# Kernel optimization log

Hardware: AMD Instinct MI355X
Metric: run time of the kernel (lower is better)

## Reference

```python
import jax, jax.numpy as jnp
import numpy as np
import math

NUM_LEVEL = 16
LEVEL_DIM = 2
BASE_RES = 16
LOG2_T = 19
LEVEL_SCALE = 1.38191288
N_POINTS = 262144

_PRIMES = np.array([1, 2654435761, 805459861], dtype=np.uint32)  # tiny-cuda-nn hash primes
_CORNERS = np.array([[(c >> d) & 1 for d in range(3)] for c in range(8)], dtype=np.uint32)  # [8,3]


def _grid_meta():
    # mirrors GridEncoder.get_grid_info: per-level table offsets (aligned to 8)
    max_len = 2 ** LOG2_T
    offs = []
    off = 0
    for i in range(NUM_LEVEL):
        res = int(np.ceil(BASE_RES * LEVEL_SCALE ** i))
        p = min(max_len, res ** 3)
        p = int(np.ceil(p / 8) * 8)
        offs.append(off)
        off += p
    offs.append(off)
    return offs


def setup_inputs() -> dict:
    key = jax.random.key(0)
    k1, k2 = jax.random.split(key)
    offs = _grid_meta()
    # raw coords in [-1, 1); forward maps (x+1)/2 -> [0, 1)
    input_means = jax.random.uniform(k1, (N_POINTS, 3), dtype=jnp.float32) * 2.0 - 1.0
    # embeddings.data.uniform_(-0.01, 0.01)
    embeddings = jax.random.uniform(k2, (offs[-1], LEVEL_DIM), dtype=jnp.float32) * 0.02 - 0.01
    return {"input_means": input_means, "embeddings": embeddings}


def _encode(input_means, embeddings):
    x = (input_means + 1.0) / 2.0  # [N,3] in [0,1]
    offs = _grid_meta()
    lg_scale = math.log2(LEVEL_SCALE)
    corners = jnp.asarray(_CORNERS)  # [8,3]
    primes = jnp.asarray(_PRIMES)    # [3]
    outs = []
    for l in range(NUM_LEVEL):
        hsize = offs[l + 1] - offs[l]                    # table rows this level
        scale = 2.0 ** (l * lg_scale) * BASE_RES - 1.0   # align_corners=True
        res = int(math.ceil(scale)) + 1                  # grid resolution
        table = embeddings[offs[l]:offs[l + 1]]          # [hsize, C]
        pos = x * scale                                  # align_corners -> no +0.5
        pg = jnp.floor(pos)
        frac = pos - pg                                  # [N,3]
        pgu = pg.astype(jnp.uint32)
        cpos = pgu[:, None, :] + corners[None]           # [N,8,3] corner coords
        if res ** 3 > hsize:
            # hashed level: xor of coord*prime (uint32 wraparound)
            h = cpos * primes
            idx = h[..., 0] ^ h[..., 1] ^ h[..., 2]
        else:
            # dense (tiled) level
            r = jnp.uint32(res)
            idx = cpos[..., 0] + cpos[..., 1] * r + cpos[..., 2] * r * r
        idx = (idx % jnp.uint32(hsize)).astype(jnp.int32)
        feats = table[idx]                               # [N,8,C] gather
        w = jnp.where(corners[None] == 1, frac[:, None, :], 1.0 - frac[:, None, :]).prod(-1)  # [N,8]
        outs.append(jnp.einsum('nk,nkc->nc', w, feats))  # trilinear interp
    # matches ot_encod.permute(1,0,2).reshape(N, L*C): level-major feature concat
    return jnp.concatenate(outs, axis=-1)                # [N, L*C]


def reference(input_means, embeddings):
    return _encode(input_means, embeddings)
```

## Files before the change

### kernel.cpp

```cpp
#include <hip/hip_runtime.h>
#include <cmath>

#define NPTS 262144
#define NLVL 16
#define NDENSE 5
#define NHASH 11
#define HASH_MASK 0x7FFFFu

#define PPT 2
#define CHUNK (256 * PPT)
#define CHUNKS_PER_LVL (NPTS / CHUNK)
#define TOTAL_UNITS (NHASH * CHUNKS_PER_LVL)
#define UNITS_PER_XCD (TOTAL_UNITS / 8)

typedef float vf2 __attribute__((ext_vector_type(2)));
typedef float vf4 __attribute__((ext_vector_type(4)));

struct MetaD { float scale[NDENSE]; unsigned off[NDENSE]; unsigned res[NDENSE]; };
struct MetaH { float scale[NHASH]; unsigned off[NHASH]; };

__device__ __forceinline__ vf2 hash_level(
    const float* __restrict__ emb, unsigned off, float s,
    float x, float y, float z)
{
    const float px = x * s, py = y * s, pz = z * s;
    const float gx = floorf(px), gy = floorf(py), gz = floorf(pz);
    const float fx = px - gx, fy = py - gy, fz = pz - gz;
    const unsigned ix = (unsigned)gx, iy = (unsigned)gy, iz = (unsigned)gz;

    const unsigned hy0 = iy * 2654435761u, hy1 = hy0 + 2654435761u;
    const unsigned hz0 = iz * 805459861u,  hz1 = hz0 + 805459861u;
    const unsigned hyz[4] = {hy0 ^ hz0, hy1 ^ hz0, hy0 ^ hz1, hy1 ^ hz1};

    const float wy0 = 1.0f - fy, wz0 = 1.0f - fz;
    const float wc[4] = {wy0 * wz0, fy * wz0, wy0 * fz, fy * fz};
    const float wx0 = 1.0f - fx;

    const vf2* __restrict__ emb2 = (const vf2*)emb;
    const vf4* __restrict__ emb4 = (const vf4*)emb;

    float a0 = 0.0f, a1 = 0.0f;
    if ((ix & 1u) == 0u) {
#pragma unroll
        for (int c = 0; c < 4; ++c) {
            const unsigned i0 = (ix ^ hyz[c]) & HASH_MASK;
            const vf4 f = emb4[(off + (i0 & ~1u)) >> 1];
            const bool sw = (i0 & 1u);
            const float c0x = sw ? f.z : f.x, c0y = sw ? f.w : f.y;
            const float c1x = sw ? f.x : f.z, c1y = sw ? f.y : f.w;
            a0 += wc[c] * (wx0 * c0x + fx * c1x);
            a1 += wc[c] * (wx0 * c0y + fx * c1y);
        }
    } else {
#pragma unroll
        for (int c = 0; c < 4; ++c) {
            const unsigned i0 = (ix        ^ hyz[c]) & HASH_MASK;
            const unsigned i1 = ((ix + 1u) ^ hyz[c]) & HASH_MASK;
            const vf2 f0 = emb2[off + i0];
            const vf2 f1 = emb2[off + i1];
            a0 += wc[c] * (wx0 * f0.x + fx * f1.x);
            a1 += wc[c] * (wx0 * f0.y + fx * f1.y);
        }
    }
    vf2 r; r.x = a0; r.y = a1;
    return r;
}

__global__ __launch_bounds__(256) void enc_hash(
    const float* __restrict__ means, const float* __restrict__ emb,
    float* __restrict__ dst, int lvl_major, MetaH meta)
{
    const unsigned b   = blockIdx.x;
    const unsigned g   = (b & 7u) * UNITS_PER_XCD + (b >> 3);
    const unsigned il  = g >> 9;
    const unsigned chk = g & 511u;

    const float sc     = meta.scale[il];
    const unsigned off = meta.off[il];
    const unsigned lvl = il + NDENSE;

    const unsigned p0 = chk * CHUNK + threadIdx.x;
    vf2* __restrict__ dst2 = (vf2*)dst;

#pragma unroll
    for (int pp = 0; pp < PPT; ++pp) {
        const unsigned p = p0 + (unsigned)pp * 256u;
        const float x = (means[3 * p + 0] + 1.0f) * 0.5f;
        const float y = (means[3 * p + 1] + 1.0f) * 0.5f;
        const float z = (means[3 * p + 2] + 1.0f) * 0.5f;
        const vf2 a = hash_level(emb, off, sc, x, y, z);
        if (lvl_major) {
            __builtin_nontemporal_store(a, &dst2[(size_t)il * NPTS + p]);
        } else {
            dst2[(size_t)p * NLVL + lvl] = a;
        }
    }
}

__global__ __launch_bounds__(256) void finalize(
    const float* __restrict__ means, const float* __restrict__ emb,
    const float* __restrict__ ws, float* __restrict__ out, MetaD meta)
{
    const int p = blockIdx.x * 256 + threadIdx.x;
    const vf2* __restrict__ ws2 = (const vf2*)ws;

    vf2 h0  = __builtin_nontemporal_load(&ws2[(size_t)0  * NPTS + p]);
    vf2 h1  = __builtin_nontemporal_load(&ws2[(size_t)1  * NPTS + p]);
    vf2 h2  = __builtin_nontemporal_load(&ws2[(size_t)2  * NPTS + p]);
    vf2 h3  = __builtin_nontemporal_load(&ws2[(size_t)3  * NPTS + p]);
    vf2 h4  = __builtin_nontemporal_load(&ws2[(size_t)4  * NPTS + p]);
    vf2 h5  = __builtin_nontemporal_load(&ws2[(size_t)5  * NPTS + p]);
    vf2 h6  = __builtin_nontemporal_load(&ws2[(size_t)6  * NPTS + p]);
    vf2 h7  = __builtin_nontemporal_load(&ws2[(size_t)7  * NPTS + p]);
    vf2 h8  = __builtin_nontemporal_load(&ws2[(size_t)8  * NPTS + p]);
    vf2 h9  = __builtin_nontemporal_load(&ws2[(size_t)9  * NPTS + p]);
    vf2 h10 = __builtin_nontemporal_load(&ws2[(size_t)10 * NPTS + p]);

    const float x = (means[3 * p + 0] + 1.0f) * 0.5f;
    const float y = (means[3 * p + 1] + 1.0f) * 0.5f;
    const float z = (means[3 * p + 2] + 1.0f) * 0.5f;

    const vf2* __restrict__ emb2 = (const vf2*)emb;

    vf2 d[NDENSE];
#pragma unroll
    for (int l = 0; l < NDENSE; ++l) {
        const float s      = meta.scale[l];
        const unsigned off = meta.off[l];
        const unsigned r   = meta.res[l];

        const float px = x * s, py = y * s, pz = z * s;
        const float gx = floorf(px), gy = floorf(py), gz = floorf(pz);
        const float fx = px - gx, fy = py - gy, fz = pz - gz;
        const unsigned ix = (unsigned)gx, iy = (unsigned)gy, iz = (unsigned)gz;

        const unsigned base = ix + iy * r + iz * r * r + off;
        const unsigned dy = r, dz = r * r;

        vf2 f[8];
        f[0] = emb2[base];           f[1] = emb2[base + 1];
        f[2] = emb2[base + dy];      f[3] = emb2[base + dy + 1];
        f[4] = emb2[base + dz];      f[5] = emb2[base + dz + 1];
        f[6] = emb2[base + dz + dy]; f[7] = emb2[base + dz + dy + 1];

        const float wx0 = 1.0f - fx, wy0 = 1.0f - fy, wz0 = 1.0f - fz;
        const float w00 = wz0 * wy0, w01 = wz0 * fy, w10 = fz * wy0, w11 = fz * fy;
        d[l].x = w00 * (wx0 * f[0].x + fx * f[1].x) + w01 * (wx0 * f[2].x + fx * f[3].x)
               + w10 * (wx0 * f[4].x + fx * f[5].x) + w11 * (wx0 * f[6].x + fx * f[7].x);
        d[l].y = w00 * (wx0 * f[0].y + fx * f[1].y) + w01 * (wx0 * f[2].y + fx * f[3].y)
               + w10 * (wx0 * f[4].y + fx * f[5].y) + w11 * (wx0 * f[6].y + fx * f[7].y);
    }

    float* o = out + (size_t)p * (2 * NLVL);
    vf4 v;
    v.x = d[0].x; v.y = d[0].y; v.z = d[1].x; v.w = d[1].y;
    __builtin_nontemporal_store(v, (vf4*)(o + 0));
    v.x = d[2].x; v.y = d[2].y; v.z = d[3].x; v.w = d[3].y;
    __builtin_nontemporal_store(v, (vf4*)(o + 4));
    v.x = d[4].x; v.y = d[4].y; v.z = h0.x;  v.w = h0.y;
    __builtin_nontemporal_store(v, (vf4*)(o + 8));
    v.x = h1.x; v.y = h1.y; v.z = h2.x; v.w = h2.y;
    __builtin_nontemporal_store(v, (vf4*)(o + 12));
    v.x = h3.x; v.y = h3.y; v.z = h4.x; v.w = h4.y;
    __builtin_nontemporal_store(v, (vf4*)(o + 16));
    v.x = h5.x; v.y = h5.y; v.z = h6.x; v.w = h6.y;
    __builtin_nontemporal_store(v, (vf4*)(o + 20));
    v.x = h7.x; v.y = h7.y; v.z = h8.x; v.w = h8.y;
    __builtin_nontemporal_store(v, (vf4*)(o + 24));
    v.x = h9.x; v.y = h9.y; v.z = h10.x; v.w = h10.y;
    __builtin_nontemporal_store(v, (vf4*)(o + 28));
}

__global__ __launch_bounds__(256) void enc_dense_direct(
    const float* __restrict__ means, const float* __restrict__ emb,
    float* __restrict__ dst, MetaD meta)
{
    const int p = blockIdx.x * 256 + threadIdx.x;
    const int l = blockIdx.y;

    const float x = (means[3 * p + 0] + 1.0f) * 0.5f;
    const float y = (means[3 * p + 1] + 1.0f) * 0.5f;
    const float z = (means[3 * p + 2] + 1.0f) * 0.5f;

    const float s      = meta.scale[l];
    const unsigned off = meta.off[l];
    const unsigned r   = meta.res[l];

    const float px = x * s, py = y * s, pz = z * s;
    const float gx = floorf(px), gy = floorf(py), gz = floorf(pz);
    const float fx = px - gx, fy = py - gy, fz = pz - gz;
    const unsigned ix = (unsigned)gx, iy = (unsigned)gy, iz = (unsigned)gz;

    const unsigned base = ix + iy * r + iz * r * r + off;
    const unsigned dy = r, dz = r * r;

    const vf2* __restrict__ emb2 = (const vf2*)emb;
    vf2 f[8];
    f[0] = emb2[base];           f[1] = emb2[base + 1];
    f[2] = emb2[base + dy];      f[3] = emb2[base + dy + 1];
    f[4] = emb2[base + dz];      f[5] = emb2[base + dz + 1];
    f[6] = emb2[base + dz + dy]; f[7] = emb2[base + dz + dy + 1];

    const float wx0 = 1.0f - fx, wy0 = 1.0f - fy, wz0 = 1.0f - fz;
    const float w00 = wz0 * wy0, w01 = wz0 * fy, w10 = fz * wy0, w11 = fz * fy;
    vf2 a;
    a.x = w00 * (wx0 * f[0].x + fx * f[1].x) + w01 * (wx0 * f[2].x + fx * f[3].x)
        + w10 * (wx0 * f[4].x + fx * f[5].x) + w11 * (wx0 * f[6].x + fx * f[7].x);
    a.y = w00 * (wx0 * f[0].y + fx * f[1].y) + w01 * (wx0 * f[2].y + fx * f[3].y)
        + w10 * (wx0 * f[4].y + fx * f[5].y) + w11 * (wx0 * f[6].y + fx * f[7].y);

    ((vf2*)dst)[(size_t)p * NLVL + l] = a;
}

extern "C" void kernel_launch(void* const* d_in, const int* in_sizes, int n_in,
                              void* d_out, int out_size, void* d_ws, size_t ws_size,
                              hipStream_t stream)
{
    const float* means = (const float*)d_in[0];
    const float* emb   = (const float*)d_in[1];
    float* out         = (float*)d_out;

    MetaD md;
    MetaH mh;
    const double lg = log2(1.38191288);
    unsigned off = 0;
    for (int l = 0; l < NLVL; ++l) {
        const double scale_d = pow(2.0, (double)l * lg) * 16.0 - 1.0;
        const unsigned res_enc = (unsigned)ceil(scale_d) + 1u;

        const double gres_d = ceil(16.0 * pow(1.38191288, (double)l));
        unsigned long long r3 = (unsigned long long)gres_d;
        r3 = r3 * r3 * r3;
        unsigned long long pl = r3 < (1ull << 19) ? r3 : (1ull << 19);
        pl = (pl + 7ull) / 8ull * 8ull;

        if (l < NDENSE) {
            md.scale[l] = (float)scale_d;
            md.off[l]   = off;
            md.res[l]   = res_enc;
        } else {
            mh.scale[l - NDENSE] = (float)scale_d;
            mh.off[l - NDENSE]   = off;
        }
        off += (unsigned)pl;
    }

    const size_t ws_needed = (size_t)NHASH * NPTS * sizeof(vf2);
    if (ws_size >= ws_needed) {
        float* ws = (float*)d_ws;
        enc_hash<<<TOTAL_UNITS, 256, 0, stream>>>(means, emb, ws, 1, mh);
        finalize<<<NPTS / 256, 256, 0, stream>>>(means, emb, ws, out, md);
    } else {
        enc_hash<<<TOTAL_UNITS, 256, 0, stream>>>(means, emb, out, 0, mh);
        enc_dense_direct<<<dim3(NPTS / 256, NDENSE, 1), 256, 0, stream>>>(means, emb, out, md);
    }
}
```

Before: 222.1 us.

## Move dense levels into the main encode kernel; finalize becomes a pure transpose

Dense-level interpolation moves out of the per-point finalize kernel and into the main encode grid as extra blocks. The finalize step becomes a plain transpose of a 16-level workspace into the level-interleaved output. This spreads the dense gathers across many more blocks and lets them overlap with the hash-level work, instead of serialising five gathers per thread in finalize. The cost is a larger workspace (16 levels instead of 11) and extra write and read traffic for the dense results. The direct path is now used only when the workspace is too small.

```diff
diff --git a/kernel.cpp b/kernel.cpp
--- a/kernel.cpp
+++ b/kernel.cpp
@@ -10,14 +10,19 @@
 #define PPT 2
 #define CHUNK (256 * PPT)
 #define CHUNKS_PER_LVL (NPTS / CHUNK)
-#define TOTAL_UNITS (NHASH * CHUNKS_PER_LVL)
-#define UNITS_PER_XCD (TOTAL_UNITS / 8)
+#define HASH_UNITS (NHASH * CHUNKS_PER_LVL)
+#define UNITS_PER_XCD (HASH_UNITS / 8)
+#define DENSE_UNITS (NDENSE * CHUNKS_PER_LVL)
+#define TOTAL_UNITS (HASH_UNITS + DENSE_UNITS)
 
 typedef float vf2 __attribute__((ext_vector_type(2)));
 typedef float vf4 __attribute__((ext_vector_type(4)));
 
-struct MetaD { float scale[NDENSE]; unsigned off[NDENSE]; unsigned res[NDENSE]; };
-struct MetaH { float scale[NHASH]; unsigned off[NHASH]; };
+struct Meta {
+    float scale[NLVL];
+    unsigned off[NLVL];
+    unsigned res[NLVL];
+};
 
 __device__ __forceinline__ vf2 hash_level(
     const float* __restrict__ emb, unsigned off, float s,
@@ -66,126 +71,10 @@
     return r;
 }
 
-__global__ __launch_bounds__(256) void enc_hash(
-    const float* __restrict__ means, const float* __restrict__ emb,
-    float* __restrict__ dst, int lvl_major, MetaH meta)
-{
-    const unsigned b   = blockIdx.x;
-    const unsigned g   = (b & 7u) * UNITS_PER_XCD + (b >> 3);
-    const unsigned il  = g >> 9;
-    const unsigned chk = g & 511u;
-
-    const float sc     = meta.scale[il];
-    const unsigned off = meta.off[il];
-    const unsigned lvl = il + NDENSE;
-
-    const unsigned p0 = chk * CHUNK + threadIdx.x;
-    vf2* __restrict__ dst2 = (vf2*)dst;
-
-#pragma unroll
-    for (int pp = 0; pp < PPT; ++pp) {
-        const unsigned p = p0 + (unsigned)pp * 256u;
-        const float x = (means[3 * p + 0] + 1.0f) * 0.5f;
-        const float y = (means[3 * p + 1] + 1.0f) * 0.5f;
-        const float z = (means[3 * p + 2] + 1.0f) * 0.5f;
-        const vf2 a = hash_level(emb, off, sc, x, y, z);
-        if (lvl_major) {
-            __builtin_nontemporal_store(a, &dst2[(size_t)il * NPTS + p]);
-        } else {
-            dst2[(size_t)p * NLVL + lvl] = a;
-        }
-    }
-}
-
-__global__ __launch_bounds__(256) void finalize(
-    const float* __restrict__ means, const float* __restrict__ emb,
-    const float* __restrict__ ws, float* __restrict__ out, MetaD meta)
-{
-    const int p = blockIdx.x * 256 + threadIdx.x;
-    const vf2* __restrict__ ws2 = (const vf2*)ws;
-
-    vf2 h0  = __builtin_nontemporal_load(&ws2[(size_t)0  * NPTS + p]);
-    vf2 h1  = __builtin_nontemporal_load(&ws2[(size_t)1  * NPTS + p]);
-    vf2 h2  = __builtin_nontemporal_load(&ws2[(size_t)2  * NPTS + p]);
-    vf2 h3  = __builtin_nontemporal_load(&ws2[(size_t)3  * NPTS + p]);
-    vf2 h4  = __builtin_nontemporal_load(&ws2[(size_t)4  * NPTS + p]);
-    vf2 h5  = __builtin_nontemporal_load(&ws2[(size_t)5  * NPTS + p]);
-    vf2 h6  = __builtin_nontemporal_load(&ws2[(size_t)6  * NPTS + p]);
-    vf2 h7  = __builtin_nontemporal_load(&ws2[(size_t)7  * NPTS + p]);
-    vf2 h8  = __builtin_nontemporal_load(&ws2[(size_t)8  * NPTS + p]);
-    vf2 h9  = __builtin_nontemporal_load(&ws2[(size_t)9  * NPTS + p]);
-    vf2 h10 = __builtin_nontemporal_load(&ws2[(size_t)10 * NPTS + p]);
-
-    const float x = (means[3 * p + 0] + 1.0f) * 0.5f;
-    const float y = (means[3 * p + 1] + 1.0f) * 0.5f;
-    const float z = (means[3 * p + 2] + 1.0f) * 0.5f;
-
-    const vf2* __restrict__ emb2 = (const vf2*)emb;
-
-    vf2 d[NDENSE];
-#pragma unroll
-    for (int l = 0; l < NDENSE; ++l) {
-        const float s      = meta.scale[l];
-        const unsigned off = meta.off[l];
-        const unsigned r   = meta.res[l];
-
-        const float px = x * s, py = y * s, pz = z * s;
-        const float gx = floorf(px), gy = floorf(py), gz = floorf(pz);
-        const float fx = px - gx, fy = py - gy, fz = pz - gz;
-        const unsigned ix = (unsigned)gx, iy = (unsigned)gy, iz = (unsigned)gz;
-
-        const unsigned base = ix + iy * r + iz * r * r + off;
-        const unsigned dy = r, dz = r * r;
-
-        vf2 f[8];
-        f[0] = emb2[base];           f[1] = emb2[base + 1];
-        f[2] = emb2[base + dy];      f[3] = emb2[base + dy + 1];
-        f[4] = emb2[base + dz];      f[5] = emb2[base + dz + 1];
-        f[6] = emb2[base + dz + dy]; f[7] = emb2[base + dz + dy + 1];
-
-        const float wx0 = 1.0f - fx, wy0 = 1.0f - fy, wz0 = 1.0f - fz;
-        const float w00 = wz0 * wy0, w01 = wz0 * fy, w10 = fz * wy0, w11 = fz * fy;
-        d[l].x = w00 * (wx0 * f[0].x + fx * f[1].x) + w01 * (wx0 * f[2].x + fx * f[3].x)
-               + w10 * (wx0 * f[4].x + fx * f[5].x) + w11 * (wx0 * f[6].x + fx * f[7].x);
-        d[l].y = w00 * (wx0 * f[0].y + fx * f[1].y) + w01 * (wx0 * f[2].y + fx * f[3].y)
-               + w10 * (wx0 * f[4].y + fx * f[5].y) + w11 * (wx0 * f[6].y + fx * f[7].y);
-    }
-
-    float* o = out + (size_t)p * (2 * NLVL);
-    vf4 v;
-    v.x = d[0].x; v.y = d[0].y; v.z = d[1].x; v.w = d[1].y;
-    __builtin_nontemporal_store(v, (vf4*)(o + 0));
-    v.x = d[2].x; v.y = d[2].y; v.z = d[3].x; v.w = d[3].y;
-    __builtin_nontemporal_store(v, (vf4*)(o + 4));
-    v.x = d[4].x; v.y = d[4].y; v.z = h0.x;  v.w = h0.y;
-    __builtin_nontemporal_store(v, (vf4*)(o + 8));
-    v.x = h1.x; v.y = h1.y; v.z = h2.x; v.w = h2.y;
-    __builtin_nontemporal_store(v, (vf4*)(o + 12));
-    v.x = h3.x; v.y = h3.y; v.z = h4.x; v.w = h4.y;
-    __builtin_nontemporal_store(v, (vf4*)(o + 16));
-    v.x = h5.x; v.y = h5.y; v.z = h6.x; v.w = h6.y;
-    __builtin_nontemporal_store(v, (vf4*)(o + 20));
-    v.x = h7.x; v.y = h7.y; v.z = h8.x; v.w = h8.y;
-    __builtin_nontemporal_store(v, (vf4*)(o + 24));
-    v.x = h9.x; v.y = h9.y; v.z = h10.x; v.w = h10.y;
-    __builtin_nontemporal_store(v, (vf4*)(o + 28));
-}
-
-__global__ __launch_bounds__(256) void enc_dense_direct(
-    const float* __restrict__ means, const float* __restrict__ emb,
-    float* __restrict__ dst, MetaD meta)
-{
-    const int p = blockIdx.x * 256 + threadIdx.x;
-    const int l = blockIdx.y;
-
-    const float x = (means[3 * p + 0] + 1.0f) * 0.5f;
-    const float y = (means[3 * p + 1] + 1.0f) * 0.5f;
-    const float z = (means[3 * p + 2] + 1.0f) * 0.5f;
-
-    const float s      = meta.scale[l];
-    const unsigned off = meta.off[l];
-    const unsigned r   = meta.res[l];
-
+__device__ __forceinline__ vf2 dense_level(
+    const float* __restrict__ emb, unsigned off, unsigned r, float s,
+    float x, float y, float z)
+{
     const float px = x * s, py = y * s, pz = z * s;
     const float gx = floorf(px), gy = floorf(py), gz = floorf(pz);
     const float fx = px - gx, fy = py - gy, fz = pz - gz;
@@ -208,8 +97,100 @@
         + w10 * (wx0 * f[4].x + fx * f[5].x) + w11 * (wx0 * f[6].x + fx * f[7].x);
     a.y = w00 * (wx0 * f[0].y + fx * f[1].y) + w01 * (wx0 * f[2].y + fx * f[3].y)
         + w10 * (wx0 * f[4].y + fx * f[5].y) + w11 * (wx0 * f[6].y + fx * f[7].y);
-
-    ((vf2*)dst)[(size_t)p * NLVL + l] = a;
+    return a;
+}
+
+__global__ __launch_bounds__(256) void encode(
+    const float* __restrict__ means, const float* __restrict__ emb,
+    float* __restrict__ ws, Meta meta)
+{
+    const unsigned b = blockIdx.x;
+    unsigned lvl, chk;
+    if (b < HASH_UNITS) {
+        const unsigned g = (b & 7u) * UNITS_PER_XCD + (b >> 3);
+        lvl = NDENSE + (g >> 9);
+        chk = g & 511u;
+    } else {
+        const unsigned d = b - HASH_UNITS;
+        lvl = d >> 9;
+        chk = d & 511u;
+    }
+
+    const float sc     = meta.scale[lvl];
+    const unsigned off = meta.off[lvl];
+    const unsigned r   = meta.res[lvl];
+
+    const unsigned p0 = chk * CHUNK + threadIdx.x;
+    vf2* __restrict__ ws2 = (vf2*)ws;
+
+#pragma unroll
+    for (int pp = 0; pp < PPT; ++pp) {
+        const unsigned p = p0 + (unsigned)pp * 256u;
+        const float x = (means[3 * p + 0] + 1.0f) * 0.5f;
+        const float y = (means[3 * p + 1] + 1.0f) * 0.5f;
+        const float z = (means[3 * p + 2] + 1.0f) * 0.5f;
+
+        vf2 a;
+        if (lvl >= NDENSE) a = hash_level(emb, off, sc, x, y, z);
+        else               a = dense_level(emb, off, r, sc, x, y, z);
+
+        __builtin_nontemporal_store(a, &ws2[(size_t)lvl * NPTS + p]);
+    }
+}
+
+__global__ __launch_bounds__(256) void transpose_out(
+    const float* __restrict__ ws, float* __restrict__ out)
+{
+    const int p = blockIdx.x * 256 + threadIdx.x;
+    const vf2* __restrict__ ws2 = (const vf2*)ws;
+
+    vf2 h[NLVL];
+#pragma unroll
+    for (int l = 0; l < NLVL; ++l)
+        h[l] = ws2[(size_t)l * NPTS + p];
+
+    float* o = out + (size_t)p * (2 * NLVL);
+#pragma unroll
+    for (int k = 0; k < 8; ++k) {
+        vf4 v;
+        v.x = h[2 * k].x; v.y = h[2 * k].y; v.z = h[2 * k + 1].x; v.w = h[2 * k + 1].y;
+        __builtin_nontemporal_store(v, (vf4*)(o + 4 * k));
+    }
+}
+
+__global__ __launch_bounds__(256) void enc_hash_direct(
+    const float* __restrict__ means, const float* __restrict__ emb,
+    float* __restrict__ dst, Meta meta)
+{
+    const unsigned b   = blockIdx.x;
+    const unsigned g   = (b & 7u) * UNITS_PER_XCD + (b >> 3);
+    const unsigned lvl = NDENSE + (g >> 9);
+    const unsigned chk = g & 511u;
+    const float sc     = meta.scale[lvl];
+    const unsigned off = meta.off[lvl];
+    const unsigned p0  = chk * CHUNK + threadIdx.x;
+    vf2* __restrict__ dst2 = (vf2*)dst;
+#pragma unroll
+    for (int pp = 0; pp < PPT; ++pp) {
+        const unsigned p = p0 + (unsigned)pp * 256u;
+        const float x = (means[3 * p + 0] + 1.0f) * 0.5f;
+        const float y = (means[3 * p + 1] + 1.0f) * 0.5f;
+        const float z = (means[3 * p + 2] + 1.0f) * 0.5f;
+        dst2[(size_t)p * NLVL + lvl] = hash_level(emb, off, sc, x, y, z);
+    }
+}
+
+__global__ __launch_bounds__(256) void enc_dense_direct(
+    const float* __restrict__ means, const float* __restrict__ emb,
+    float* __restrict__ dst, Meta meta)
+{
+    const int p = blockIdx.x * 256 + threadIdx.x;
+    const int l = blockIdx.y;
+    const float x = (means[3 * p + 0] + 1.0f) * 0.5f;
+    const float y = (means[3 * p + 1] + 1.0f) * 0.5f;
+    const float z = (means[3 * p + 2] + 1.0f) * 0.5f;
+    ((vf2*)dst)[(size_t)p * NLVL + l] =
+        dense_level(emb, meta.off[l], meta.res[l], meta.scale[l], x, y, z);
 }
 
 extern "C" void kernel_launch(void* const* d_in, const int* in_sizes, int n_in,
@@ -220,13 +201,13 @@
     const float* emb   = (const float*)d_in[1];
     float* out         = (float*)d_out;
 
-    MetaD md;
-    MetaH mh;
+    Meta m;
     const double lg = log2(1.38191288);
     unsigned off = 0;
     for (int l = 0; l < NLVL; ++l) {
         const double scale_d = pow(2.0, (double)l * lg) * 16.0 - 1.0;
-        const unsigned res_enc = (unsigned)ceil(scale_d) + 1u;
+        m.scale[l] = (float)scale_d;
+        m.res[l]   = (unsigned)ceil(scale_d) + 1u;
 
         const double gres_d = ceil(16.0 * pow(1.38191288, (double)l));
         unsigned long long r3 = (unsigned long long)gres_d;
@@ -234,24 +215,17 @@
         unsigned long long pl = r3 < (1ull << 19) ? r3 : (1ull << 19);
         pl = (pl + 7ull) / 8ull * 8ull;
 
-        if (l < NDENSE) {
-            md.scale[l] = (float)scale_d;
-            md.off[l]   = off;
-            md.res[l]   = res_enc;
-        } else {
-            mh.scale[l - NDENSE] = (float)scale_d;
-            mh.off[l - NDENSE]   = off;
-        }
+        m.off[l] = off;
         off += (unsigned)pl;
     }
 
-    const size_t ws_needed = (size_t)NHASH * NPTS * sizeof(vf2);
-    if (ws_size >= ws_needed) {
+    const size_t ws_full = (size_t)NLVL * NPTS * sizeof(vf2);
+    if (ws_size >= ws_full) {
         float* ws = (float*)d_ws;
-        enc_hash<<<TOTAL_UNITS, 256, 0, stream>>>(means, emb, ws, 1, mh);
-        finalize<<<NPTS / 256, 256, 0, stream>>>(means, emb, ws, out, md);
+        encode<<<TOTAL_UNITS, 256, 0, stream>>>(means, emb, ws, m);
+        transpose_out<<<NPTS / 256, 256, 0, stream>>>(ws, out);
     } else {
-        enc_hash<<<TOTAL_UNITS, 256, 0, stream>>>(means, emb, out, 0, mh);
-        enc_dense_direct<<<dim3(NPTS / 256, NDENSE, 1), 256, 0, stream>>>(means, emb, out, md);
-    }
-}
+        enc_hash_direct<<<HASH_UNITS, 256, 0, stream>>>(means, emb, out, m);
+        enc_dense_direct<<<dim3(NPTS / 256, NDENSE, 1), 256, 0, stream>>>(means, emb, out, m);
+    }
+}
```

New measurement: 251.1 us. +13.0%, slower.
